# Kernel tuning notes

Hardware: AMD Instinct MI355X
Metric: run time of the kernel (lower is better)

The kernel has to match this reference:

```python
import jax, jax.numpy as jnp
import numpy as np

H = 512

def _lstm_cell(x, h, c, Wih, Whh, bih, bhh):
    # torch LSTM gate order: i, f, g, o
    g = x @ Wih.T + bih + h @ Whh.T + bhh  # (B, 4H)
    i, f, gg, o = jnp.split(g, 4, axis=-1)
    i = jax.nn.sigmoid(i); f = jax.nn.sigmoid(f)
    gg = jnp.tanh(gg);     o = jax.nn.sigmoid(o)
    c_new = f * c + i * gg
    h_new = o * jnp.tanh(c_new)
    return h_new, c_new

def setup_inputs() -> dict:
    key = jax.random.key(0)
    ks = jax.random.split(key, 16)
    B, S, F = 32, 128, 2
    s = 1.0 / np.sqrt(H)
    u = lambda k, shape: jax.random.uniform(k, shape, jnp.float32, -s, s)
    return {
        "inputs": jax.random.normal(ks[0], (B, S, F), jnp.float32),
        "Wp": u(ks[1], (H, F)), "bp": u(ks[2], (H,)),
        "enc_Wih": u(ks[3], (4 * H, H)), "enc_Whh": u(ks[4], (4 * H, H)),
        "enc_bih": u(ks[5], (4 * H,)),   "enc_bhh": u(ks[6], (4 * H,)),
        "dec_Wih": u(ks[7], (4 * H, H)), "dec_Whh": u(ks[8], (4 * H, H)),
        "dec_bih": u(ks[9], (4 * H,)),   "dec_bhh": u(ks[10], (4 * H,)),
        "W1": u(ks[11], (H, H)), "W2": u(ks[12], (H, H)),
        "v": u(ks[13], (H,)),
    }

def reference(inputs, Wp, bp, enc_Wih, enc_Whh, enc_bih, enc_bhh,
              dec_Wih, dec_Whh, dec_bih, dec_bhh, W1, W2, v):
    B, S, _ = inputs.shape
    trg_len = S
    x = inputs @ Wp.T + bp  # (B, S, H) input projection

    # --- encoder LSTM over time ---
    h0 = jnp.zeros((B, H), inputs.dtype)
    c0 = jnp.zeros((B, H), inputs.dtype)
    def enc_step(carry, xt):
        h, c = carry
        h, c = _lstm_cell(xt, h, c, enc_Wih, enc_Whh, enc_bih, enc_bhh)
        return (h, c), h
    (h, c), enc_hs = jax.lax.scan(enc_step, (h0, c0), jnp.swapaxes(x, 0, 1))
    encoder_outputs = jnp.swapaxes(enc_hs, 0, 1)  # (B, S, H)

    # loop-invariant encoder projection (hoisted; identical math)
    enc_proj = encoder_outputs @ W1.T  # (B, S, H)

    # NOTE: the original module never updates its mask (stays all-False),
    # so masking is a no-op and is faithfully omitted.
    dec_in0 = jnp.zeros((B, H), inputs.dtype)
    batch_idx = jnp.arange(B)

    def dec_step(carry, _):
        h, c, dec_in = carry
        h, c = _lstm_cell(dec_in, h, c, dec_Wih, dec_Whh, dec_bih, dec_bhh)
        dec_proj = h @ W2.T  # (B, H)
        scores = jnp.einsum('bsh,h->bs', jnp.tanh(enc_proj + dec_proj[:, None, :]), v)
        log_probs = jax.nn.log_softmax(scores, axis=-1)  # (B, S)
        top_idx = jnp.argmax(log_probs, axis=-1)  # (B,)
        next_in = encoder_outputs[batch_idx, top_idx]  # (B, H)
        return (h, c, next_in), log_probs

    _, all_lp = jax.lax.scan(dec_step, (h, c, dec_in0), None, length=trg_len)
    return jnp.swapaxes(all_lp, 0, 1)  # (B, trg_len, S)
```

## Files before the change

kernel.cpp:

```cpp
#include <hip/hip_runtime.h>
#include <math.h>

static constexpr int H   = 512;
static constexpr int B   = 32;
static constexpr int S   = 128;
static constexpr int G4  = 2048;
static constexpr int UPS = 64;
static constexpr int RPS = 256;
static constexpr int NSL = 8;

static constexpr size_t OFF_E   = 0;
static constexpr size_t SZ_E    = (size_t)B * S * G4;
static constexpr size_t OFF_EO  = OFF_E + SZ_E;
static constexpr size_t SZ_EO   = (size_t)B * S * H;
static constexpr size_t OFF_PT  = OFF_EO + SZ_EO;
static constexpr size_t SZ_PT   = (size_t)B * H * S;
static constexpr size_t OFF_WPE = OFF_PT + SZ_PT;
static constexpr size_t SZ_WP   = (size_t)NSL * H * RPS;
static constexpr size_t OFF_WPD = OFF_WPE + SZ_WP;
static constexpr size_t OFF_W2T = OFF_WPD + SZ_WP;
static constexpr size_t OFF_HB  = OFF_W2T + (size_t)H * H;
static constexpr size_t OFF_CB  = OFF_HB + (size_t)B * 2 * H;
static constexpr size_t OFF_PS  = OFF_CB + (size_t)B * H;
static constexpr size_t OFF_M1  = OFF_PS + (size_t)B * 512;
static constexpr size_t OFF_BE  = OFF_M1 + (size_t)G4 * 2;
static constexpr size_t OFF_DB  = OFF_BE + G4;
static constexpr size_t OFF_END = OFF_DB + G4;
static constexpr int CTRL_U32 = (256 + 256 + 128 + 32) * 32;

__device__ __forceinline__ float sigm(float x){
  float e = __expf(-x);
  return 1.0f / (1.0f + e);
}
__device__ __forceinline__ float tanh_(float x){
  float e = __expf(2.0f * x);
  return 1.0f - 2.0f / (1.0f + e);
}

__device__ __forceinline__ float cloadf(const float* p){
  union { unsigned u; float f; } c;
  c.u = __hip_atomic_load((const unsigned*)p, __ATOMIC_RELAXED,
                          __HIP_MEMORY_SCOPE_AGENT);
  return c.f;
}
__device__ __forceinline__ float2 cload2(const float* p){
  union { unsigned long long u; float2 f; } c;
  c.u = __hip_atomic_load((const unsigned long long*)p, __ATOMIC_RELAXED,
                          __HIP_MEMORY_SCOPE_AGENT);
  return c.f;
}
__device__ __forceinline__ void cstore2(float* p, float a, float b){
  union { unsigned long long u; float2 f; } c;
  c.f = make_float2(a, b);
  __hip_atomic_store((unsigned long long*)p, c.u, __ATOMIC_RELAXED,
                     __HIP_MEMORY_SCOPE_AGENT);
}
__device__ __forceinline__ unsigned cloadu(const unsigned* p){
  return __hip_atomic_load(p, __ATOMIC_RELAXED, __HIP_MEMORY_SCOPE_AGENT);
}
__device__ __forceinline__ void cstoreu(unsigned* p, unsigned v){
  __hip_atomic_store(p, v, __ATOMIC_RELAXED, __HIP_MEMORY_SCOPE_AGENT);
}

__global__ __launch_bounds__(256) void prep_misc(
    const float* __restrict__ eWih, const float* __restrict__ Wp,
    const float* __restrict__ bp,  const float* __restrict__ ebih,
    const float* __restrict__ ebhh, const float* __restrict__ dbih,
    const float* __restrict__ dbhh,
    float* __restrict__ M1, float* __restrict__ bias_e, float* __restrict__ dbias)
{
  int c = blockIdx.x * 256 + threadIdx.x;
  const float* wr = eWih + (size_t)c * H;
  float m0 = 0.f, m1 = 0.f, mb = 0.f;
  for (int k = 0; k < H; k += 4){
    float4 w  = *(const float4*)(wr + k);
    float4 p0 = *(const float4*)(Wp + (size_t)k * 2);
    float4 p1 = *(const float4*)(Wp + (size_t)(k + 2) * 2);
    float4 bb = *(const float4*)(bp + k);
    m0 += w.x*p0.x + w.y*p0.z + w.z*p1.x + w.w*p1.z;
    m1 += w.x*p0.y + w.y*p0.w + w.z*p1.y + w.w*p1.w;
    mb += w.x*bb.x + w.y*bb.y + w.z*bb.z + w.w*bb.w;
  }
  M1[(size_t)c*2]   = m0;
  M1[(size_t)c*2+1] = m1;
  bias_e[c] = ebih[c] + ebhh[c] + mb;
  dbias[c]  = dbih[c] + dbhh[c];
}

__global__ __launch_bounds__(256) void efill(
    const float* __restrict__ inp, const float* __restrict__ M1,
    const float* __restrict__ be, float* __restrict__ E)
{
  size_t i = (size_t)blockIdx.x * 256 + threadIdx.x;
  int c = (int)(i & 2047);
  int t = (int)((i >> 11) & 127);
  int b = (int)(i >> 18);
  float x0 = inp[((size_t)b * S + t) * 2 + 0];
  float x1 = inp[((size_t)b * S + t) * 2 + 1];
  E[i] = M1[(size_t)c*2] * x0 + M1[(size_t)c*2+1] * x1 + be[c];
}

__global__ __launch_bounds__(256) void pack_whh(
    const float* __restrict__ Whh, float* __restrict__ WP)
{
  size_t i = (size_t)blockIdx.x * 256 + threadIdx.x;
  int p = (int)(i & 255);
  int k = (int)((i >> 8) & 511);
  int j = (int)(i >> 17);
  int g = p >> 6, u = p & 63;
  int r = g * 512 + j * UPS + u;
  WP[i] = Whh[(size_t)r * H + k];
}

__global__ __launch_bounds__(256) void transpose_k(
    const float* __restrict__ in, float* __restrict__ out, int R, int K)
{
  __shared__ float tile[32][33];
  int r0 = blockIdx.y * 32, k0 = blockIdx.x * 32;
  int tx = threadIdx.x & 31, ty = threadIdx.x >> 5;
  #pragma unroll
  for (int j = 0; j < 4; ++j)
    tile[ty + 8*j][tx] = in[(size_t)(r0 + ty + 8*j) * K + k0 + tx];
  __syncthreads();
  #pragma unroll
  for (int j = 0; j < 4; ++j)
    out[(size_t)(k0 + ty + 8*j) * R + r0 + tx] = tile[tx][ty + 8*j];
}

template<int LAYOUT>
__global__ __launch_bounds__(256) void gemm_nt(
    const float* __restrict__ A, const float* __restrict__ Bm,
    const float* __restrict__ bias, float* __restrict__ C,
    int M, int N, int K)
{
  __shared__ float As[16][68];
  __shared__ float Bs[16][68];
  int tid = threadIdx.x;
  int bm = blockIdx.y * 64, bn = blockIdx.x * 64;
  int tm = (tid & 15) * 4, tn = (tid >> 4) * 4;
  float acc[4][4] = {};
  int r  = tid >> 2;
  int kq = (tid & 3) * 4;
  for (int k0 = 0; k0 < K; k0 += 16){
    float4 a = *(const float4*)(A  + (size_t)(bm + r) * K + k0 + kq);
    float4 b = *(const float4*)(Bm + (size_t)(bn + r) * K + k0 + kq);
    __syncthreads();
    As[kq+0][r] = a.x; As[kq+1][r] = a.y; As[kq+2][r] = a.z; As[kq+3][r] = a.w;
    Bs[kq+0][r] = b.x; Bs[kq+1][r] = b.y; Bs[kq+2][r] = b.z; Bs[kq+3][r] = b.w;
    __syncthreads();
    #pragma unroll
    for (int kk = 0; kk < 16; ++kk){
      float4 av = *(const float4*)(&As[kk][tm]);
      float4 bv = *(const float4*)(&Bs[kk][tn]);
      acc[0][0] += av.x*bv.x; acc[0][1] += av.x*bv.y; acc[0][2] += av.x*bv.z; acc[0][3] += av.x*bv.w;
      acc[1][0] += av.y*bv.x; acc[1][1] += av.y*bv.y; acc[1][2] += av.y*bv.z; acc[1][3] += av.y*bv.w;
      acc[2][0] += av.z*bv.x; acc[2][1] += av.z*bv.y; acc[2][2] += av.z*bv.z; acc[2][3] += av.z*bv.w;
      acc[3][0] += av.w*bv.x; acc[3][1] += av.w*bv.y; acc[3][2] += av.w*bv.z; acc[3][3] += av.w*bv.w;
    }
  }
  #pragma unroll
  for (int i = 0; i < 4; ++i){
    int m = bm + tm + i;
    #pragma unroll
    for (int j = 0; j < 4; ++j){
      int n = bn + tn + j;
      float vv = acc[i][j] + (bias ? bias[n] : 0.f);
      if (LAYOUT == 0) C[(size_t)m * N + n] = vv;
      else             C[((size_t)(m >> 7) * 512 + n) * 128 + (m & 127)] = vv;
    }
  }
}

__global__ __launch_bounds__(256) void encoder_kernel(
    const float* __restrict__ WP,
    const float* __restrict__ E,
    float* __restrict__ hb,
    float* __restrict__ c_buf,
    float* __restrict__ enc_out,
    unsigned* __restrict__ htags)
{
  __shared__ float hsh[H];
  __shared__ float gpart[4][RPS];
  __shared__ float gfin[4][UPS];
  __shared__ float hloc[UPS];
  const int tid = threadIdx.x, bk = blockIdx.x;
  const int b = bk >> 3, j = bk & 7;
  const int u0 = j * UPS;
  const float* wp = WP + (size_t)j * H * RPS;
  unsigned* myhtags = htags + (size_t)b * 8 * 32;
  const int ph = tid >> 6, c4 = tid & 63;
  float creg = 0.f;
  for (int t = 0; t < S; ++t){
    if (t > 0 && tid < 8){
      while (cloadu(myhtags + tid * 32) < (unsigned)t){}
    }
    __syncthreads();
    { float2 q = cload2(hb + ((size_t)b * 2 + ((t + 1) & 1)) * H + 2 * tid);
      hsh[2*tid] = q.x; hsh[2*tid + 1] = q.y; }
    __syncthreads();
    float4 acc = {0.f, 0.f, 0.f, 0.f};
    const float* wq = wp + ph * RPS + c4 * 4;
    #pragma unroll 4
    for (int kk = 0; kk < 128; ++kk){
      float hv = hsh[4*kk + ph];
      float4 w = *(const float4*)(wq + (size_t)kk * 4 * RPS);
      acc.x = fmaf(w.x, hv, acc.x); acc.y = fmaf(w.y, hv, acc.y);
      acc.z = fmaf(w.z, hv, acc.z); acc.w = fmaf(w.w, hv, acc.w);
    }
    *(float4*)&gpart[ph][c4 * 4] = acc;
    __syncthreads();
    if (tid < 64){
      float4 s0 = *(const float4*)&gpart[0][tid*4];
      float4 s1 = *(const float4*)&gpart[1][tid*4];
      float4 s2 = *(const float4*)&gpart[2][tid*4];
      float4 s3 = *(const float4*)&gpart[3][tid*4];
      int g = tid >> 4, uu = (tid & 15) * 4;
      float4 e = *(const float4*)(E + ((size_t)b * S + t) * G4 + g * 512 + u0 + uu);
      float4 s; s.x = s0.x+s1.x+s2.x+s3.x + e.x; s.y = s0.y+s1.y+s2.y+s3.y + e.y;
      s.z = s0.z+s1.z+s2.z+s3.z + e.z; s.w = s0.w+s1.w+s2.w+s3.w + e.w;
      *(float4*)&gfin[g][uu] = s;
    }
    __syncthreads();
    if (tid < UPS){
      float gi = gfin[0][tid], gf = gfin[1][tid], gg = gfin[2][tid], go = gfin[3][tid];
      creg = sigm(gf) * creg + sigm(gi) * tanh_(gg);
      hloc[tid] = sigm(go) * tanh_(creg);
    }
    __syncthreads();
    if (tid < 32){
      float h0 = hloc[2*tid], h1 = hloc[2*tid + 1];
      cstore2(hb + ((size_t)b * 2 + (t & 1)) * H + u0 + 2*tid, h0, h1);
      *(float2*)(enc_out + ((size_t)b * S + t) * H + u0 + 2*tid) = make_float2(h0, h1);
    }
    __syncthreads();
    if (tid == 0) cstoreu(myhtags + j * 32, (unsigned)(t + 1));
  }
  if (tid < UPS) c_buf[(size_t)b * H + u0 + tid] = creg;
}

__global__ __launch_bounds__(256) void decoder_kernel(
    const float* __restrict__ WP,
    const float* __restrict__ D,
    const float* __restrict__ dbias,
    const float* __restrict__ W2T,
    const float* __restrict__ Pt,
    const float* __restrict__ vvec,
    const float* __restrict__ c_buf,
    const float* __restrict__ enc_out,
    float* __restrict__ hb,
    float* __restrict__ psbuf,
    unsigned* __restrict__ htags,
    unsigned* __restrict__ pstags,
    unsigned* __restrict__ tops,
    float* __restrict__ out)
{
  const int tid = threadIdx.x, bk = blockIdx.x;
  if (bk < 256){
    __shared__ float hsh[H];
    __shared__ float gpart[4][RPS];
    __shared__ float gfin[4][UPS];
    __shared__ float hloc[UPS];
    __shared__ int   topsh;
    const int b = bk >> 3, j = bk & 7;
    const int u0 = j * UPS;
    const float* wp = WP + (size_t)j * H * RPS;
    unsigned* myhtags = htags + (size_t)b * 8 * 32;
    const unsigned* mytop = tops + (size_t)b * 32;
    const int ph = tid >> 6, c4 = tid & 63;
    float creg = (tid < UPS) ? c_buf[(size_t)b * H + u0 + tid] : 0.f;
    if (tid < 32){
      float2 hv = *(const float2*)(enc_out + ((size_t)b * S + (S-1)) * H + u0 + 2*tid);
      cstore2(hb + ((size_t)b * 2 + 1) * H + u0 + 2*tid, hv.x, hv.y);
    }
    __syncthreads();
    if (tid == 0) cstoreu(myhtags + j * 32, 1u);
    for (int t = 0; t < S; ++t){
      if (tid < 8){
        while (cloadu(myhtags + tid * 32) < (unsigned)(t + 1)) __builtin_amdgcn_s_sleep(1);
      }
      __syncthreads();
      { float2 q = cload2(hb + ((size_t)b * 2 + ((t + 1) & 1)) * H + 2 * tid);
        hsh[2*tid] = q.x; hsh[2*tid + 1] = q.y; }
      __syncthreads();
      float4 acc = {0.f, 0.f, 0.f, 0.f};
      const float* wq = wp + ph * RPS + c4 * 4;
      #pragma unroll 4
      for (int kk = 0; kk < 128; ++kk){
        float hv = hsh[4*kk + ph];
        float4 w = *(const float4*)(wq + (size_t)kk * 4 * RPS);
        acc.x = fmaf(w.x, hv, acc.x); acc.y = fmaf(w.y, hv, acc.y);
        acc.z = fmaf(w.z, hv, acc.z); acc.w = fmaf(w.w, hv, acc.w);
      }
      *(float4*)&gpart[ph][c4 * 4] = acc;
      if (t > 0 && tid == 0){
        unsigned vt;
        do { vt = cloadu(mytop); } while ((vt >> 8) != (unsigned)t);
        topsh = (int)(vt & 255u);
      }
      __syncthreads();
      if (tid < 64){
        float4 s0 = *(const float4*)&gpart[0][tid*4];
        float4 s1 = *(const float4*)&gpart[1][tid*4];
        float4 s2 = *(const float4*)&gpart[2][tid*4];
        float4 s3 = *(const float4*)&gpart[3][tid*4];
        int g = tid >> 4, uu = (tid & 15) * 4;
        const float* xr = (t == 0) ? dbias : D + ((size_t)b * S + topsh) * G4;
        float4 e = *(const float4*)(xr + g * 512 + u0 + uu);
        float4 s; s.x = s0.x+s1.x+s2.x+s3.x + e.x; s.y = s0.y+s1.y+s2.y+s3.y + e.y;
        s.z = s0.z+s1.z+s2.z+s3.z + e.z; s.w = s0.w+s1.w+s2.w+s3.w + e.w;
        *(float4*)&gfin[g][uu] = s;
      }
      __syncthreads();
      if (tid < UPS){
        float gi = gfin[0][tid], gf = gfin[1][tid], gg = gfin[2][tid], go = gfin[3][tid];
        creg = sigm(gf) * creg + sigm(gi) * tanh_(gg);
        hloc[tid] = sigm(go) * tanh_(creg);
      }
      __syncthreads();
      if (tid < 32)
        cstore2(hb + ((size_t)b * 2 + (t & 1)) * H + u0 + 2*tid,
                hloc[2*tid], hloc[2*tid + 1]);
      __syncthreads();
      if (tid == 0) cstoreu(myhtags + j * 32, (unsigned)(t + 2));
    }
  } else if (bk < 384){
    __shared__ float hsh[H];
    __shared__ float dps[2][128];
    __shared__ float dpl[128];
    __shared__ float vsh2[128];
    __shared__ float pspart[2][128];
    const int b = (bk - 256) >> 2, q = (bk - 256) & 3;
    const unsigned* myhtags = htags + (size_t)b * 8 * 32;
    unsigned* mytag = pstags + (size_t)(b * 4 + q) * 32;
    if (tid < 128) vsh2[tid] = vvec[q * 128 + tid];
    for (int tau = 0; tau < S; ++tau){
      if (tid < 8){
        while (cloadu(myhtags + tid * 32) < (unsigned)(tau + 2)) __builtin_amdgcn_s_sleep(1);
      }
      __syncthreads();
      { float2 qq = cload2(hb + ((size_t)b * 2 + (tau & 1)) * H + 2 * tid);
        hsh[2*tid] = qq.x; hsh[2*tid + 1] = qq.y; }
      __syncthreads();
      {
        int nl = tid & 127, kh = tid >> 7;
        const float* w = W2T + (size_t)(kh * 256) * H + q * 128 + nl;
        float a = 0.f;
        #pragma unroll 8
        for (int k2 = 0; k2 < 256; ++k2)
          a = fmaf(w[(size_t)k2 * H], hsh[kh * 256 + k2], a);
        dps[kh][nl] = a;
      }
      __syncthreads();
      if (tid < 128) dpl[tid] = dps[0][tid] + dps[1][tid];
      __syncthreads();
      {
        int s = tid & 127, nh = tid >> 7;
        const float* Pp = Pt + ((size_t)b * H + q * 128 + nh * 64) * S + s;
        float cs = 0.f;
        #pragma unroll 4
        for (int n = 0; n < 64; ++n){
          float x = Pp[(size_t)n * S] + dpl[nh * 64 + n];
          cs = fmaf(vsh2[nh * 64 + n], tanh_(x), cs);
        }
        pspart[nh][s] = cs;
      }
      __syncthreads();
      if (tid < 64)
        cstore2(psbuf + ((size_t)b * 4 + q) * 128 + 2 * tid,
                pspart[0][2*tid] + pspart[1][2*tid],
                pspart[0][2*tid+1] + pspart[1][2*tid+1]);
      __syncthreads();
      if (tid == 0) cstoreu(mytag, (unsigned)(tau + 1));
    }
  } else {
    __shared__ float wm[2]; __shared__ int wi[2]; __shared__ float wsum[2];
    const int b = bk - 384;
    unsigned* mytop = tops + (size_t)b * 32;
    for (int t = 0; t < S; ++t){
      if (tid < 4){
        const unsigned* L = pstags + (size_t)(b * 4 + tid) * 32;
        while (cloadu(L) < (unsigned)(t + 1)) __builtin_amdgcn_s_sleep(1);
      }
      __syncthreads();
      float sc = 0.f;
      if (tid < 128){
        const float* pp = psbuf + (size_t)b * 512 + tid;
        sc = cloadf(pp) + cloadf(pp + 128) + cloadf(pp + 256) + cloadf(pp + 384);
        float mv = sc; int mi = tid;
        #pragma unroll
        for (int off = 32; off > 0; off >>= 1){
          float ov = __shfl_xor(mv, off, 64);
          int   oi = __shfl_xor(mi, off, 64);
          if (ov > mv || (ov == mv && oi < mi)){ mv = ov; mi = oi; }
        }
        if ((tid & 63) == 0){ wm[tid >> 6] = mv; wi[tid >> 6] = mi; }
      }
      __syncthreads();
      float mglob; int am;
      { float m0 = wm[0], m1 = wm[1];
        if (m1 > m0 || (m1 == m0 && wi[1] < wi[0])){ mglob = m1; am = wi[1]; }
        else { mglob = m0; am = wi[0]; } }
      if (tid == 0) cstoreu(mytop, ((unsigned)(t + 1) << 8) | (unsigned)am);
      if (tid < 128){
        float se = __expf(sc - mglob);
        float ss = se;
        #pragma unroll
        for (int off = 32; off > 0; off >>= 1) ss += __shfl_xor(ss, off, 64);
        if ((tid & 63) == 0) wsum[tid >> 6] = ss;
      }
      __syncthreads();
      if (tid < 128){
        float lse = __logf(wsum[0] + wsum[1]);
        out[((size_t)b * S + t) * S + tid] = sc - mglob - lse;
      }
      __syncthreads();
    }
  }
}

extern "C" void kernel_launch(void* const* d_in, const int* in_sizes, int n_in,
                              void* d_out, int out_size, void* d_ws, size_t ws_size,
                              hipStream_t stream) {
  const float* inputs  = (const float*)d_in[0];
  const float* Wp      = (const float*)d_in[1];
  const float* bp      = (const float*)d_in[2];
  const float* eWih    = (const float*)d_in[3];
  const float* eWhh    = (const float*)d_in[4];
  const float* ebih    = (const float*)d_in[5];
  const float* ebhh    = (const float*)d_in[6];
  const float* dWih    = (const float*)d_in[7];
  const float* dWhh    = (const float*)d_in[8];
  const float* dbih    = (const float*)d_in[9];
  const float* dbhh    = (const float*)d_in[10];
  const float* W1      = (const float*)d_in[11];
  const float* W2      = (const float*)d_in[12];
  const float* v       = (const float*)d_in[13];
  float* out = (float*)d_out;

  float* ws = (float*)d_ws;
  float* E       = ws + OFF_E;
  float* enc_out = ws + OFF_EO;
  float* Pt      = ws + OFF_PT;
  float* WPe     = ws + OFF_WPE;
  float* WPd     = ws + OFF_WPD;
  float* W2T     = ws + OFF_W2T;
  float* hb      = ws + OFF_HB;
  float* c_buf   = ws + OFF_CB;
  float* psbuf   = ws + OFF_PS;
  float* M1      = ws + OFF_M1;
  float* bias_e  = ws + OFF_BE;
  float* dbias   = ws + OFF_DB;
  unsigned* enc_htags = (unsigned*)(ws + OFF_END);
  unsigned* dec_htags = enc_htags + 256 * 32;
  unsigned* pstags    = dec_htags + 256 * 32;
  unsigned* tops      = pstags + 128 * 32;

  hipMemsetAsync(hb, 0, (size_t)B * 2 * H * sizeof(float), stream);
  hipMemsetAsync(enc_htags, 0, CTRL_U32 * sizeof(unsigned), stream);

  prep_misc<<<G4 / 256, 256, 0, stream>>>(eWih, Wp, bp, ebih, ebhh, dbih, dbhh,
                                          M1, bias_e, dbias);
  efill<<<(int)(SZ_E / 256), 256, 0, stream>>>(inputs, M1, bias_e, E);
  pack_whh<<<(int)(SZ_WP / 256), 256, 0, stream>>>(eWhh, WPe);
  pack_whh<<<(int)(SZ_WP / 256), 256, 0, stream>>>(dWhh, WPd);
  { dim3 g(H / 32, H / 32); transpose_k<<<g, 256, 0, stream>>>(W2, W2T, H, H); }

  encoder_kernel<<<256, 256, 0, stream>>>(WPe, E, hb, c_buf, enc_out, enc_htags);

  float* D = E;
  { dim3 grid(G4 / 64, (B * S) / 64);
    gemm_nt<0><<<grid, 256, 0, stream>>>(enc_out, dWih, dbias, D, B * S, G4, H); }
  { dim3 grid(H / 64, (B * S) / 64);
    gemm_nt<1><<<grid, 256, 0, stream>>>(enc_out, W1, nullptr, Pt, B * S, H, H); }

  decoder_kernel<<<416, 256, 0, stream>>>(WPd, D, dbias, W2T, Pt, v, c_buf,
                                          enc_out, hb, psbuf,
                                          dec_htags, pstags, tops, out);
  (void)in_sizes; (void)n_in; (void)out_size; (void)ws_size;
}
```

Before: 2.959 ms.

## Batch four sequences per block in encoder/decoder to reuse recurrent weights

Each LSTM block now handles four batch rows at once, so every Whh weight slice loaded from memory is reused four times. The encoder grid drops from 256 to 64 blocks and the decoder from 416 to 104. The argmax moves into the LSTM blocks, which read the double-buffered scores themselves, and the log-softmax blocks only write output and signal back through a new tag. This shortens the cross-block dependency chain and cuts weight traffic, but uses far fewer CUs and puts more serial work on each block.

```diff
diff --git a/kernel.cpp b/kernel.cpp
--- a/kernel.cpp
+++ b/kernel.cpp
@@ -8,6 +8,8 @@
 static constexpr int UPS = 64;
 static constexpr int RPS = 256;
 static constexpr int NSL = 8;
+static constexpr int BPG = 4;
+static constexpr int NG  = 8;
 
 static constexpr size_t OFF_E   = 0;
 static constexpr size_t SZ_E    = (size_t)B * S * G4;
@@ -22,11 +24,11 @@
 static constexpr size_t OFF_HB  = OFF_W2T + (size_t)H * H;
 static constexpr size_t OFF_CB  = OFF_HB + (size_t)B * 2 * H;
 static constexpr size_t OFF_PS  = OFF_CB + (size_t)B * H;
-static constexpr size_t OFF_M1  = OFF_PS + (size_t)B * 512;
+static constexpr size_t OFF_M1  = OFF_PS + (size_t)B * 2 * 512;
 static constexpr size_t OFF_BE  = OFF_M1 + (size_t)G4 * 2;
 static constexpr size_t OFF_DB  = OFF_BE + G4;
 static constexpr size_t OFF_END = OFF_DB + G4;
-static constexpr int CTRL_U32 = (256 + 256 + 128 + 32) * 32;
+static constexpr int CTRL_U32 = (64 + 64 + 32 + 8) * 32;
 
 __device__ __forceinline__ float sigm(float x){
   float e = __expf(-x);
@@ -42,6 +44,11 @@
   c.u = __hip_atomic_load((const unsigned*)p, __ATOMIC_RELAXED,
                           __HIP_MEMORY_SCOPE_AGENT);
   return c.f;
+}
+__device__ __forceinline__ void cstoref(float* p, float v){
+  union { unsigned u; float f; } c; c.f = v;
+  __hip_atomic_store((unsigned*)p, c.u, __ATOMIC_RELAXED,
+                     __HIP_MEMORY_SCOPE_AGENT);
 }
 __device__ __forceinline__ float2 cload2(const float* p){
   union { unsigned long long u; float2 f; } c;
@@ -171,6 +178,15 @@
   }
 }
 
+__device__ __forceinline__ void stage_h4(const float* hb, int b0, int par,
+                                         float* hsh, int tid){
+  #pragma unroll
+  for (int bb = 0; bb < BPG; ++bb){
+    float2 q = cload2(hb + ((size_t)(b0 + bb) * 2 + par) * H + 2 * tid);
+    hsh[bb * H + 2 * tid] = q.x; hsh[bb * H + 2 * tid + 1] = q.y;
+  }
+}
+
 __global__ __launch_bounds__(256) void encoder_kernel(
     const float* __restrict__ WP,
     const float* __restrict__ E,
@@ -179,63 +195,55 @@
     float* __restrict__ enc_out,
     unsigned* __restrict__ htags)
 {
-  __shared__ float hsh[H];
-  __shared__ float gpart[4][RPS];
-  __shared__ float gfin[4][UPS];
-  __shared__ float hloc[UPS];
+  __shared__ float hsh[BPG * H];
+  __shared__ float gpart[4][BPG][RPS];
   const int tid = threadIdx.x, bk = blockIdx.x;
-  const int b = bk >> 3, j = bk & 7;
-  const int u0 = j * UPS;
+  const int g = bk >> 3, j = bk & 7;
+  const int b0 = g * BPG, u0 = j * UPS;
   const float* wp = WP + (size_t)j * H * RPS;
-  unsigned* myhtags = htags + (size_t)b * 8 * 32;
+  unsigned* myhtags = htags + (size_t)g * 8 * 32;
   const int ph = tid >> 6, c4 = tid & 63;
+  const int bb = tid >> 6, u = tid & 63;
   float creg = 0.f;
   for (int t = 0; t < S; ++t){
     if (t > 0 && tid < 8){
-      while (cloadu(myhtags + tid * 32) < (unsigned)t){}
-    }
-    __syncthreads();
-    { float2 q = cload2(hb + ((size_t)b * 2 + ((t + 1) & 1)) * H + 2 * tid);
-      hsh[2*tid] = q.x; hsh[2*tid + 1] = q.y; }
-    __syncthreads();
-    float4 acc = {0.f, 0.f, 0.f, 0.f};
+      while (cloadu(myhtags + tid * 32) < (unsigned)t) __builtin_amdgcn_s_sleep(1);
+    }
+    __syncthreads();
+    stage_h4(hb, b0, (t + 1) & 1, hsh, tid);
+    __syncthreads();
+    float4 a0 = {0,0,0,0}, a1 = {0,0,0,0}, a2 = {0,0,0,0}, a3 = {0,0,0,0};
     const float* wq = wp + ph * RPS + c4 * 4;
     #pragma unroll 4
     for (int kk = 0; kk < 128; ++kk){
-      float hv = hsh[4*kk + ph];
+      int k = 4 * kk + ph;
       float4 w = *(const float4*)(wq + (size_t)kk * 4 * RPS);
-      acc.x = fmaf(w.x, hv, acc.x); acc.y = fmaf(w.y, hv, acc.y);
-      acc.z = fmaf(w.z, hv, acc.z); acc.w = fmaf(w.w, hv, acc.w);
-    }
-    *(float4*)&gpart[ph][c4 * 4] = acc;
-    __syncthreads();
-    if (tid < 64){
-      float4 s0 = *(const float4*)&gpart[0][tid*4];
-      float4 s1 = *(const float4*)&gpart[1][tid*4];
-      float4 s2 = *(const float4*)&gpart[2][tid*4];
-      float4 s3 = *(const float4*)&gpart[3][tid*4];
-      int g = tid >> 4, uu = (tid & 15) * 4;
-      float4 e = *(const float4*)(E + ((size_t)b * S + t) * G4 + g * 512 + u0 + uu);
-      float4 s; s.x = s0.x+s1.x+s2.x+s3.x + e.x; s.y = s0.y+s1.y+s2.y+s3.y + e.y;
-      s.z = s0.z+s1.z+s2.z+s3.z + e.z; s.w = s0.w+s1.w+s2.w+s3.w + e.w;
-      *(float4*)&gfin[g][uu] = s;
-    }
-    __syncthreads();
-    if (tid < UPS){
-      float gi = gfin[0][tid], gf = gfin[1][tid], gg = gfin[2][tid], go = gfin[3][tid];
+      float h0 = hsh[k], h1 = hsh[H + k], h2 = hsh[2*H + k], h3 = hsh[3*H + k];
+      a0.x = fmaf(w.x,h0,a0.x); a0.y = fmaf(w.y,h0,a0.y); a0.z = fmaf(w.z,h0,a0.z); a0.w = fmaf(w.w,h0,a0.w);
+      a1.x = fmaf(w.x,h1,a1.x); a1.y = fmaf(w.y,h1,a1.y); a1.z = fmaf(w.z,h1,a1.z); a1.w = fmaf(w.w,h1,a1.w);
+      a2.x = fmaf(w.x,h2,a2.x); a2.y = fmaf(w.y,h2,a2.y); a2.z = fmaf(w.z,h2,a2.z); a2.w = fmaf(w.w,h2,a2.w);
+      a3.x = fmaf(w.x,h3,a3.x); a3.y = fmaf(w.y,h3,a3.y); a3.z = fmaf(w.z,h3,a3.z); a3.w = fmaf(w.w,h3,a3.w);
+    }
+    *(float4*)&gpart[ph][0][c4 * 4] = a0;
+    *(float4*)&gpart[ph][1][c4 * 4] = a1;
+    *(float4*)&gpart[ph][2][c4 * 4] = a2;
+    *(float4*)&gpart[ph][3][c4 * 4] = a3;
+    __syncthreads();
+    {
+      const float* xr = E + ((size_t)(b0 + bb) * S + t) * G4;
+      float gi = gpart[0][bb][      u] + gpart[1][bb][      u] + gpart[2][bb][      u] + gpart[3][bb][      u] + xr[       u0 + u];
+      float gf = gpart[0][bb][ 64 + u] + gpart[1][bb][ 64 + u] + gpart[2][bb][ 64 + u] + gpart[3][bb][ 64 + u] + xr[512  + u0 + u];
+      float gg = gpart[0][bb][128 + u] + gpart[1][bb][128 + u] + gpart[2][bb][128 + u] + gpart[3][bb][128 + u] + xr[1024 + u0 + u];
+      float go = gpart[0][bb][192 + u] + gpart[1][bb][192 + u] + gpart[2][bb][192 + u] + gpart[3][bb][192 + u] + xr[1536 + u0 + u];
       creg = sigm(gf) * creg + sigm(gi) * tanh_(gg);
-      hloc[tid] = sigm(go) * tanh_(creg);
-    }
-    __syncthreads();
-    if (tid < 32){
-      float h0 = hloc[2*tid], h1 = hloc[2*tid + 1];
-      cstore2(hb + ((size_t)b * 2 + (t & 1)) * H + u0 + 2*tid, h0, h1);
-      *(float2*)(enc_out + ((size_t)b * S + t) * H + u0 + 2*tid) = make_float2(h0, h1);
+      float hn = sigm(go) * tanh_(creg);
+      cstoref(hb + ((size_t)(b0 + bb) * 2 + (t & 1)) * H + u0 + u, hn);
+      enc_out[((size_t)(b0 + bb) * S + t) * H + u0 + u] = hn;
     }
     __syncthreads();
     if (tid == 0) cstoreu(myhtags + j * 32, (unsigned)(t + 1));
   }
-  if (tid < UPS) c_buf[(size_t)b * H + u0 + tid] = creg;
+  c_buf[(size_t)(b0 + bb) * H + u0 + u] = creg;
 }
 
 __global__ __launch_bounds__(256) void decoder_kernel(
@@ -251,27 +259,22 @@
     float* __restrict__ psbuf,
     unsigned* __restrict__ htags,
     unsigned* __restrict__ pstags,
-    unsigned* __restrict__ tops,
+    unsigned* __restrict__ otags,
     float* __restrict__ out)
 {
   const int tid = threadIdx.x, bk = blockIdx.x;
-  if (bk < 256){
-    __shared__ float hsh[H];
-    __shared__ float gpart[4][RPS];
-    __shared__ float gfin[4][UPS];
-    __shared__ float hloc[UPS];
-    __shared__ int   topsh;
-    const int b = bk >> 3, j = bk & 7;
-    const int u0 = j * UPS;
+  if (bk < 64){
+    __shared__ float hsh[BPG * H];
+    __shared__ float gpart[4][BPG][RPS];
+    const int g = bk >> 3, j = bk & 7;
+    const int b0 = g * BPG, u0 = j * UPS;
     const float* wp = WP + (size_t)j * H * RPS;
-    unsigned* myhtags = htags + (size_t)b * 8 * 32;
-    const unsigned* mytop = tops + (size_t)b * 32;
+    unsigned* myhtags = htags + (size_t)g * 8 * 32;
     const int ph = tid >> 6, c4 = tid & 63;
-    float creg = (tid < UPS) ? c_buf[(size_t)b * H + u0 + tid] : 0.f;
-    if (tid < 32){
-      float2 hv = *(const float2*)(enc_out + ((size_t)b * S + (S-1)) * H + u0 + 2*tid);
-      cstore2(hb + ((size_t)b * 2 + 1) * H + u0 + 2*tid, hv.x, hv.y);
-    }
+    const int bb = tid >> 6, u = tid & 63;
+    float creg = c_buf[(size_t)(b0 + bb) * H + u0 + u];
+    cstoref(hb + ((size_t)(b0 + bb) * 2 + 1) * H + u0 + u,
+            enc_out[((size_t)(b0 + bb) * S + (S-1)) * H + u0 + u]);
     __syncthreads();
     if (tid == 0) cstoreu(myhtags + j * 32, 1u);
     for (int t = 0; t < S; ++t){
@@ -279,141 +282,157 @@
         while (cloadu(myhtags + tid * 32) < (unsigned)(t + 1)) __builtin_amdgcn_s_sleep(1);
       }
       __syncthreads();
-      { float2 q = cload2(hb + ((size_t)b * 2 + ((t + 1) & 1)) * H + 2 * tid);
-        hsh[2*tid] = q.x; hsh[2*tid + 1] = q.y; }
-      __syncthreads();
-      float4 acc = {0.f, 0.f, 0.f, 0.f};
+      stage_h4(hb, b0, (t + 1) & 1, hsh, tid);
+      __syncthreads();
+      float4 a0 = {0,0,0,0}, a1 = {0,0,0,0}, a2 = {0,0,0,0}, a3 = {0,0,0,0};
       const float* wq = wp + ph * RPS + c4 * 4;
       #pragma unroll 4
       for (int kk = 0; kk < 128; ++kk){
-        float hv = hsh[4*kk + ph];
+        int k = 4 * kk + ph;
         float4 w = *(const float4*)(wq + (size_t)kk * 4 * RPS);
-        acc.x = fmaf(w.x, hv, acc.x); acc.y = fmaf(w.y, hv, acc.y);
-        acc.z = fmaf(w.z, hv, acc.z); acc.w = fmaf(w.w, hv, acc.w);
-      }
-      *(float4*)&gpart[ph][c4 * 4] = acc;
-      if (t > 0 && tid == 0){
-        unsigned vt;
-        do { vt = cloadu(mytop); } while ((vt >> 8) != (unsigned)t);
-        topsh = (int)(vt & 255u);
-      }
-      __syncthreads();
-      if (tid < 64){
-        float4 s0 = *(const float4*)&gpart[0][tid*4];
-        float4 s1 = *(const float4*)&gpart[1][tid*4];
-        float4 s2 = *(const float4*)&gpart[2][tid*4];
-        float4 s3 = *(const float4*)&gpart[3][tid*4];
-        int g = tid >> 4, uu = (tid & 15) * 4;
-        const float* xr = (t == 0) ? dbias : D + ((size_t)b * S + topsh) * G4;
-        float4 e = *(const float4*)(xr + g * 512 + u0 + uu);
-        float4 s; s.x = s0.x+s1.x+s2.x+s3.x + e.x; s.y = s0.y+s1.y+s2.y+s3.y + e.y;
-        s.z = s0.z+s1.z+s2.z+s3.z + e.z; s.w = s0.w+s1.w+s2.w+s3.w + e.w;
-        *(float4*)&gfin[g][uu] = s;
-      }
-      __syncthreads();
-      if (tid < UPS){
-        float gi = gfin[0][tid], gf = gfin[1][tid], gg = gfin[2][tid], go = gfin[3][tid];
-        creg = sigm(gf) * creg + sigm(gi) * tanh_(gg);
-        hloc[tid] = sigm(go) * tanh_(creg);
-      }
-      __syncthreads();
-      if (tid < 32)
-        cstore2(hb + ((size_t)b * 2 + (t & 1)) * H + u0 + 2*tid,
-                hloc[2*tid], hloc[2*tid + 1]);
-      __syncthreads();
-      if (tid == 0) cstoreu(myhtags + j * 32, (unsigned)(t + 2));
-    }
-  } else if (bk < 384){
-    __shared__ float hsh[H];
-    __shared__ float dps[2][128];
-    __shared__ float dpl[128];
-    __shared__ float vsh2[128];
-    __shared__ float pspart[2][128];
-    const int b = (bk - 256) >> 2, q = (bk - 256) & 3;
-    const unsigned* myhtags = htags + (size_t)b * 8 * 32;
-    unsigned* mytag = pstags + (size_t)(b * 4 + q) * 32;
-    if (tid < 128) vsh2[tid] = vvec[q * 128 + tid];
-    for (int tau = 0; tau < S; ++tau){
-      if (tid < 8){
-        while (cloadu(myhtags + tid * 32) < (unsigned)(tau + 2)) __builtin_amdgcn_s_sleep(1);
-      }
-      __syncthreads();
-      { float2 qq = cload2(hb + ((size_t)b * 2 + (tau & 1)) * H + 2 * tid);
-        hsh[2*tid] = qq.x; hsh[2*tid + 1] = qq.y; }
-      __syncthreads();
-      {
-        int nl = tid & 127, kh = tid >> 7;
-        const float* w = W2T + (size_t)(kh * 256) * H + q * 128 + nl;
-        float a = 0.f;
-        #pragma unroll 8
-        for (int k2 = 0; k2 < 256; ++k2)
-          a = fmaf(w[(size_t)k2 * H], hsh[kh * 256 + k2], a);
-        dps[kh][nl] = a;
-      }
-      __syncthreads();
-      if (tid < 128) dpl[tid] = dps[0][tid] + dps[1][tid];
-      __syncthreads();
-      {
-        int s = tid & 127, nh = tid >> 7;
-        const float* Pp = Pt + ((size_t)b * H + q * 128 + nh * 64) * S + s;
-        float cs = 0.f;
-        #pragma unroll 4
-        for (int n = 0; n < 64; ++n){
-          float x = Pp[(size_t)n * S] + dpl[nh * 64 + n];
-          cs = fmaf(vsh2[nh * 64 + n], tanh_(x), cs);
-        }
-        pspart[nh][s] = cs;
-      }
-      __syncthreads();
-      if (tid < 64)
-        cstore2(psbuf + ((size_t)b * 4 + q) * 128 + 2 * tid,
-                pspart[0][2*tid] + pspart[1][2*tid],
-                pspart[0][2*tid+1] + pspart[1][2*tid+1]);
-      __syncthreads();
-      if (tid == 0) cstoreu(mytag, (unsigned)(tau + 1));
-    }
-  } else {
-    __shared__ float wm[2]; __shared__ int wi[2]; __shared__ float wsum[2];
-    const int b = bk - 384;
-    unsigned* mytop = tops + (size_t)b * 32;
-    for (int t = 0; t < S; ++t){
-      if (tid < 4){
-        const unsigned* L = pstags + (size_t)(b * 4 + tid) * 32;
-        while (cloadu(L) < (unsigned)(t + 1)) __builtin_amdgcn_s_sleep(1);
-      }
-      __syncthreads();
-      float sc = 0.f;
-      if (tid < 128){
-        const float* pp = psbuf + (size_t)b * 512 + tid;
-        sc = cloadf(pp) + cloadf(pp + 128) + cloadf(pp + 256) + cloadf(pp + 384);
-        float mv = sc; int mi = tid;
+        float h0 = hsh[k], h1 = hsh[H + k], h2 = hsh[2*H + k], h3 = hsh[3*H + k];
+        a0.x = fmaf(w.x,h0,a0.x); a0.y = fmaf(w.y,h0,a0.y); a0.z = fmaf(w.z,h0,a0.z); a0.w = fmaf(w.w,h0,a0.w);
+        a1.x = fmaf(w.x,h1,a1.x); a1.y = fmaf(w.y,h1,a1.y); a1.z = fmaf(w.z,h1,a1.z); a1.w = fmaf(w.w,h1,a1.w);
+        a2.x = fmaf(w.x,h2,a2.x); a2.y = fmaf(w.y,h2,a2.y); a2.z = fmaf(w.z,h2,a2.z); a2.w = fmaf(w.w,h2,a2.w);
+        a3.x = fmaf(w.x,h3,a3.x); a3.y = fmaf(w.y,h3,a3.y); a3.z = fmaf(w.z,h3,a3.z); a3.w = fmaf(w.w,h3,a3.w);
+      }
+      *(float4*)&gpart[ph][0][c4 * 4] = a0;
+      *(float4*)&gpart[ph][1][c4 * 4] = a1;
+      *(float4*)&gpart[ph][2][c4 * 4] = a2;
+      *(float4*)&gpart[ph][3][c4 * 4] = a3;
+      if (t >= 1 && tid < 4){
+        while (cloadu(pstags + (size_t)(g * 4 + tid) * 32) < (unsigned)t)
+          __builtin_amdgcn_s_sleep(1);
+      }
+      __syncthreads();
+      int top = 0;
+      if (t >= 1){
+        const float* pp = psbuf + ((size_t)(b0 + bb) * 2 + ((t + 1) & 1)) * 512;
+        float s0 = cloadf(pp + u)       + cloadf(pp + 128 + u)
+                 + cloadf(pp + 256 + u) + cloadf(pp + 384 + u);
+        float s1 = cloadf(pp + 64 + u)  + cloadf(pp + 192 + u)
+                 + cloadf(pp + 320 + u) + cloadf(pp + 448 + u);
+        float mv; int mi;
+        if (s1 > s0){ mv = s1; mi = u + 64; } else { mv = s0; mi = u; }
         #pragma unroll
         for (int off = 32; off > 0; off >>= 1){
           float ov = __shfl_xor(mv, off, 64);
           int   oi = __shfl_xor(mi, off, 64);
           if (ov > mv || (ov == mv && oi < mi)){ mv = ov; mi = oi; }
         }
-        if ((tid & 63) == 0){ wm[tid >> 6] = mv; wi[tid >> 6] = mi; }
-      }
-      __syncthreads();
-      float mglob; int am;
-      { float m0 = wm[0], m1 = wm[1];
-        if (m1 > m0 || (m1 == m0 && wi[1] < wi[0])){ mglob = m1; am = wi[1]; }
-        else { mglob = m0; am = wi[0]; } }
-      if (tid == 0) cstoreu(mytop, ((unsigned)(t + 1) << 8) | (unsigned)am);
-      if (tid < 128){
-        float se = __expf(sc - mglob);
-        float ss = se;
+        top = mi;
+      }
+      {
+        const float* xr = (t == 0) ? dbias
+                                   : D + ((size_t)(b0 + bb) * S + top) * G4;
+        float gi = gpart[0][bb][      u] + gpart[1][bb][      u] + gpart[2][bb][      u] + gpart[3][bb][      u] + xr[       u0 + u];
+        float gf = gpart[0][bb][ 64 + u] + gpart[1][bb][ 64 + u] + gpart[2][bb][ 64 + u] + gpart[3][bb][ 64 + u] + xr[512  + u0 + u];
+        float gg = gpart[0][bb][128 + u] + gpart[1][bb][128 + u] + gpart[2][bb][128 + u] + gpart[3][bb][128 + u] + xr[1024 + u0 + u];
+        float go = gpart[0][bb][192 + u] + gpart[1][bb][192 + u] + gpart[2][bb][192 + u] + gpart[3][bb][192 + u] + xr[1536 + u0 + u];
+        creg = sigm(gf) * creg + sigm(gi) * tanh_(gg);
+        float hn = sigm(go) * tanh_(creg);
+        cstoref(hb + ((size_t)(b0 + bb) * 2 + (t & 1)) * H + u0 + u, hn);
+      }
+      __syncthreads();
+      if (tid == 0) cstoreu(myhtags + j * 32, (unsigned)(t + 2));
+    }
+  } else if (bk < 96){
+    __shared__ float hsh[BPG * H];
+    __shared__ float dps[2][BPG][128];
+    __shared__ float dpl[BPG][128];
+    __shared__ float vsh[128];
+    __shared__ float psps[BPG][128];
+    const int idx = bk - 64;
+    const int g = idx >> 2, q = idx & 3;
+    const int b0 = g * BPG;
+    unsigned* myhtags = htags + (size_t)g * 8 * 32;
+    unsigned* mytag = pstags + (size_t)(g * 4 + q) * 32;
+    const unsigned* myotag = otags + (size_t)g * 32;
+    if (tid < 128) vsh[tid] = vvec[q * 128 + tid];
+    for (int tau = 0; tau < S; ++tau){
+      if (tid < 8){
+        while (cloadu(myhtags + tid * 32) < (unsigned)(tau + 2)) __builtin_amdgcn_s_sleep(1);
+      } else if (tid == 8 && tau >= 2){
+        while (cloadu(myotag) < (unsigned)(tau - 1)) __builtin_amdgcn_s_sleep(1);
+      }
+      __syncthreads();
+      stage_h4(hb, b0, tau & 1, hsh, tid);
+      __syncthreads();
+      {
+        int nl = tid & 127, kh = tid >> 7;
+        const float* w = W2T + (size_t)(kh * 256) * H + q * 128 + nl;
+        float d0 = 0.f, d1 = 0.f, d2 = 0.f, d3 = 0.f;
+        const float* h0p = hsh + kh * 256;
+        #pragma unroll 8
+        for (int k2 = 0; k2 < 256; ++k2){
+          float wv = w[(size_t)k2 * H];
+          d0 = fmaf(wv, h0p[k2],         d0);
+          d1 = fmaf(wv, h0p[H + k2],     d1);
+          d2 = fmaf(wv, h0p[2*H + k2],   d2);
+          d3 = fmaf(wv, h0p[3*H + k2],   d3);
+        }
+        dps[kh][0][nl] = d0; dps[kh][1][nl] = d1;
+        dps[kh][2][nl] = d2; dps[kh][3][nl] = d3;
+      }
+      __syncthreads();
+      { int w2 = tid;        dpl[w2 >> 7][w2 & 127] = dps[0][w2 >> 7][w2 & 127] + dps[1][w2 >> 7][w2 & 127];
+        w2 = tid + 256;      dpl[w2 >> 7][w2 & 127] = dps[0][w2 >> 7][w2 & 127] + dps[1][w2 >> 7][w2 & 127]; }
+      __syncthreads();
+      {
+        int s = tid & 127, pair = tid >> 7;
         #pragma unroll
-        for (int off = 32; off > 0; off >>= 1) ss += __shfl_xor(ss, off, 64);
-        if ((tid & 63) == 0) wsum[tid >> 6] = ss;
-      }
-      __syncthreads();
-      if (tid < 128){
-        float lse = __logf(wsum[0] + wsum[1]);
-        out[((size_t)b * S + t) * S + tid] = sc - mglob - lse;
-      }
-      __syncthreads();
+        for (int e = 0; e < 2; ++e){
+          int bb = pair + 2 * e;
+          const float* Pp = Pt + ((size_t)(b0 + bb) * H + q * 128) * S + s;
+          const float* dq = dpl[bb];
+          float cs = 0.f;
+          #pragma unroll 4
+          for (int n = 0; n < 128; ++n){
+            float x = Pp[(size_t)n * S] + dq[n];
+            cs = fmaf(vsh[n], tanh_(x), cs);
+          }
+          psps[bb][s] = cs;
+        }
+      }
+      __syncthreads();
+      {
+        int bb = tid >> 6, i = tid & 63;
+        cstore2(psbuf + ((size_t)(b0 + bb) * 2 + (tau & 1)) * 512 + q * 128 + 2 * i,
+                psps[bb][2*i], psps[bb][2*i + 1]);
+      }
+      __syncthreads();
+      if (tid == 0) cstoreu(mytag, (unsigned)(tau + 1));
+    }
+  } else {
+    const int g = bk - 96;
+    const int b0 = g * BPG;
+    unsigned* myotag = otags + (size_t)g * 32;
+    const int bb = tid >> 6, u = tid & 63;
+    for (int t = 0; t < S; ++t){
+      if (tid < 4){
+        while (cloadu(pstags + (size_t)(g * 4 + tid) * 32) < (unsigned)(t + 1))
+          __builtin_amdgcn_s_sleep(1);
+      }
+      __syncthreads();
+      const float* pp = psbuf + ((size_t)(b0 + bb) * 2 + (t & 1)) * 512;
+      float s0 = cloadf(pp + u)       + cloadf(pp + 128 + u)
+               + cloadf(pp + 256 + u) + cloadf(pp + 384 + u);
+      float s1 = cloadf(pp + 64 + u)  + cloadf(pp + 192 + u)
+               + cloadf(pp + 320 + u) + cloadf(pp + 448 + u);
+      float mv = fmaxf(s0, s1);
+      #pragma unroll
+      for (int off = 32; off > 0; off >>= 1)
+        mv = fmaxf(mv, __shfl_xor(mv, off, 64));
+      float ss = __expf(s0 - mv) + __expf(s1 - mv);
+      #pragma unroll
+      for (int off = 32; off > 0; off >>= 1)
+        ss += __shfl_xor(ss, off, 64);
+      float lse = __logf(ss);
+      float* orow = out + ((size_t)(b0 + bb) * S + t) * S;
+      orow[u]      = s0 - mv - lse;
+      orow[64 + u] = s1 - mv - lse;
+      __syncthreads();
+      if (tid == 0) cstoreu(myotag, (unsigned)(t + 1));
     }
   }
 }
@@ -451,9 +470,9 @@
   float* bias_e  = ws + OFF_BE;
   float* dbias   = ws + OFF_DB;
   unsigned* enc_htags = (unsigned*)(ws + OFF_END);
-  unsigned* dec_htags = enc_htags + 256 * 32;
-  unsigned* pstags    = dec_htags + 256 * 32;
-  unsigned* tops      = pstags + 128 * 32;
+  unsigned* dec_htags = enc_htags + 64 * 32;
+  unsigned* pstags    = dec_htags + 64 * 32;
+  unsigned* otags     = pstags + 32 * 32;
 
   hipMemsetAsync(hb, 0, (size_t)B * 2 * H * sizeof(float), stream);
   hipMemsetAsync(enc_htags, 0, CTRL_U32 * sizeof(unsigned), stream);
@@ -465,7 +484,7 @@
   pack_whh<<<(int)(SZ_WP / 256), 256, 0, stream>>>(dWhh, WPd);
   { dim3 g(H / 32, H / 32); transpose_k<<<g, 256, 0, stream>>>(W2, W2T, H, H); }
 
-  encoder_kernel<<<256, 256, 0, stream>>>(WPe, E, hb, c_buf, enc_out, enc_htags);
+  encoder_kernel<<<64, 256, 0, stream>>>(WPe, E, hb, c_buf, enc_out, enc_htags);
 
   float* D = E;
   { dim3 grid(G4 / 64, (B * S) / 64);
@@ -473,8 +492,8 @@
   { dim3 grid(H / 64, (B * S) / 64);
     gemm_nt<1><<<grid, 256, 0, stream>>>(enc_out, W1, nullptr, Pt, B * S, H, H); }
 
-  decoder_kernel<<<416, 256, 0, stream>>>(WPd, D, dbias, W2T, Pt, v, c_buf,
+  decoder_kernel<<<104, 256, 0, stream>>>(WPd, D, dbias, W2T, Pt, v, c_buf,
                                           enc_out, hb, psbuf,
-                                          dec_htags, pstags, tops, out);
+                                          dec_htags, pstags, otags, out);
   (void)in_sizes; (void)n_in; (void)out_size; (void)ws_size;
 }
```

Result: slower. 4.733 ms (+59.9%).

## Compute argmax redundantly in LSTM blocks to remove a cross-block handoff hop

Applied to the files above, without the earlier changes.

Each decoder LSTM block now reads the four partial score slices and does its own argmax, instead of waiting on a top-index tag published by a separate softmax block. This removes one inter-block signalling hop from the serial per-step critical path. The score buffer is double-buffered, and the score blocks now wait on a new output tag from the softmax block so a buffer is not overwritten before it is read. The cost is redundant argmax work across 8 blocks per batch row and extra polling.

```diff
diff --git a/kernel.cpp b/kernel.cpp
--- a/kernel.cpp
+++ b/kernel.cpp
@@ -22,7 +22,7 @@
 static constexpr size_t OFF_HB  = OFF_W2T + (size_t)H * H;
 static constexpr size_t OFF_CB  = OFF_HB + (size_t)B * 2 * H;
 static constexpr size_t OFF_PS  = OFF_CB + (size_t)B * H;
-static constexpr size_t OFF_M1  = OFF_PS + (size_t)B * 512;
+static constexpr size_t OFF_M1  = OFF_PS + (size_t)B * 2 * 512;
 static constexpr size_t OFF_BE  = OFF_M1 + (size_t)G4 * 2;
 static constexpr size_t OFF_DB  = OFF_BE + G4;
 static constexpr size_t OFF_END = OFF_DB + G4;
@@ -251,7 +251,7 @@
     float* __restrict__ psbuf,
     unsigned* __restrict__ htags,
     unsigned* __restrict__ pstags,
-    unsigned* __restrict__ tops,
+    unsigned* __restrict__ otags,
     float* __restrict__ out)
 {
   const int tid = threadIdx.x, bk = blockIdx.x;
@@ -260,12 +260,11 @@
     __shared__ float gpart[4][RPS];
     __shared__ float gfin[4][UPS];
     __shared__ float hloc[UPS];
-    __shared__ int   topsh;
+    __shared__ float wm[2]; __shared__ int wi[2];
     const int b = bk >> 3, j = bk & 7;
     const int u0 = j * UPS;
     const float* wp = WP + (size_t)j * H * RPS;
     unsigned* myhtags = htags + (size_t)b * 8 * 32;
-    const unsigned* mytop = tops + (size_t)b * 32;
     const int ph = tid >> 6, c4 = tid & 63;
     float creg = (tid < UPS) ? c_buf[(size_t)b * H + u0 + tid] : 0.f;
     if (tid < 32){
@@ -292,19 +291,34 @@
         acc.z = fmaf(w.z, hv, acc.z); acc.w = fmaf(w.w, hv, acc.w);
       }
       *(float4*)&gpart[ph][c4 * 4] = acc;
-      if (t > 0 && tid == 0){
-        unsigned vt;
-        do { vt = cloadu(mytop); } while ((vt >> 8) != (unsigned)t);
-        topsh = (int)(vt & 255u);
-      }
-      __syncthreads();
+      if (t >= 1 && tid < 4){
+        while (cloadu(pstags + (size_t)(b * 4 + tid) * 32) < (unsigned)t)
+          __builtin_amdgcn_s_sleep(1);
+      }
+      __syncthreads();
+      if (t >= 1 && tid < 128){
+        const float* pp = psbuf + ((size_t)b * 2 + ((t + 1) & 1)) * 512 + tid;
+        float sc = cloadf(pp) + cloadf(pp + 128) + cloadf(pp + 256) + cloadf(pp + 384);
+        float mv = sc; int mi = tid;
+        #pragma unroll
+        for (int off = 32; off > 0; off >>= 1){
+          float ov = __shfl_xor(mv, off, 64);
+          int   oi = __shfl_xor(mi, off, 64);
+          if (ov > mv || (ov == mv && oi < mi)){ mv = ov; mi = oi; }
+        }
+        if ((tid & 63) == 0){ wm[tid >> 6] = mv; wi[tid >> 6] = mi; }
+      }
+      __syncthreads();
+      int top = 0;
+      if (t >= 1)
+        top = (wm[1] > wm[0] || (wm[1] == wm[0] && wi[1] < wi[0])) ? wi[1] : wi[0];
       if (tid < 64){
         float4 s0 = *(const float4*)&gpart[0][tid*4];
         float4 s1 = *(const float4*)&gpart[1][tid*4];
         float4 s2 = *(const float4*)&gpart[2][tid*4];
         float4 s3 = *(const float4*)&gpart[3][tid*4];
         int g = tid >> 4, uu = (tid & 15) * 4;
-        const float* xr = (t == 0) ? dbias : D + ((size_t)b * S + topsh) * G4;
+        const float* xr = (t == 0) ? dbias : D + ((size_t)b * S + top) * G4;
         float4 e = *(const float4*)(xr + g * 512 + u0 + uu);
         float4 s; s.x = s0.x+s1.x+s2.x+s3.x + e.x; s.y = s0.y+s1.y+s2.y+s3.y + e.y;
         s.z = s0.z+s1.z+s2.z+s3.z + e.z; s.w = s0.w+s1.w+s2.w+s3.w + e.w;
@@ -332,10 +346,13 @@
     const int b = (bk - 256) >> 2, q = (bk - 256) & 3;
     const unsigned* myhtags = htags + (size_t)b * 8 * 32;
     unsigned* mytag = pstags + (size_t)(b * 4 + q) * 32;
+    const unsigned* myotag = otags + (size_t)b * 32;
     if (tid < 128) vsh2[tid] = vvec[q * 128 + tid];
     for (int tau = 0; tau < S; ++tau){
       if (tid < 8){
         while (cloadu(myhtags + tid * 32) < (unsigned)(tau + 2)) __builtin_amdgcn_s_sleep(1);
+      } else if (tid == 8 && tau >= 2){
+        while (cloadu(myotag) < (unsigned)(tau - 1)) __builtin_amdgcn_s_sleep(1);
       }
       __syncthreads();
       { float2 qq = cload2(hb + ((size_t)b * 2 + (tau & 1)) * H + 2 * tid);
@@ -366,44 +383,36 @@
       }
       __syncthreads();
       if (tid < 64)
-        cstore2(psbuf + ((size_t)b * 4 + q) * 128 + 2 * tid,
+        cstore2(psbuf + ((size_t)b * 2 + (tau & 1)) * 512 + q * 128 + 2 * tid,
                 pspart[0][2*tid] + pspart[1][2*tid],
                 pspart[0][2*tid+1] + pspart[1][2*tid+1]);
       __syncthreads();
       if (tid == 0) cstoreu(mytag, (unsigned)(tau + 1));
     }
   } else {
-    __shared__ float wm[2]; __shared__ int wi[2]; __shared__ float wsum[2];
+    __shared__ float wm2[2]; __shared__ float wsum[2];
     const int b = bk - 384;
-    unsigned* mytop = tops + (size_t)b * 32;
+    unsigned* myotag = otags + (size_t)b * 32;
     for (int t = 0; t < S; ++t){
       if (tid < 4){
-        const unsigned* L = pstags + (size_t)(b * 4 + tid) * 32;
-        while (cloadu(L) < (unsigned)(t + 1)) __builtin_amdgcn_s_sleep(1);
+        while (cloadu(pstags + (size_t)(b * 4 + tid) * 32) < (unsigned)(t + 1))
+          __builtin_amdgcn_s_sleep(1);
       }
       __syncthreads();
       float sc = 0.f;
       if (tid < 128){
-        const float* pp = psbuf + (size_t)b * 512 + tid;
+        const float* pp = psbuf + ((size_t)b * 2 + (t & 1)) * 512 + tid;
         sc = cloadf(pp) + cloadf(pp + 128) + cloadf(pp + 256) + cloadf(pp + 384);
-        float mv = sc; int mi = tid;
+        float mv = sc;
         #pragma unroll
-        for (int off = 32; off > 0; off >>= 1){
-          float ov = __shfl_xor(mv, off, 64);
-          int   oi = __shfl_xor(mi, off, 64);
-          if (ov > mv || (ov == mv && oi < mi)){ mv = ov; mi = oi; }
-        }
-        if ((tid & 63) == 0){ wm[tid >> 6] = mv; wi[tid >> 6] = mi; }
-      }
-      __syncthreads();
-      float mglob; int am;
-      { float m0 = wm[0], m1 = wm[1];
-        if (m1 > m0 || (m1 == m0 && wi[1] < wi[0])){ mglob = m1; am = wi[1]; }
-        else { mglob = m0; am = wi[0]; } }
-      if (tid == 0) cstoreu(mytop, ((unsigned)(t + 1) << 8) | (unsigned)am);
+        for (int off = 32; off > 0; off >>= 1)
+          mv = fmaxf(mv, __shfl_xor(mv, off, 64));
+        if ((tid & 63) == 0) wm2[tid >> 6] = mv;
+      }
+      __syncthreads();
+      float mglob = fmaxf(wm2[0], wm2[1]);
       if (tid < 128){
-        float se = __expf(sc - mglob);
-        float ss = se;
+        float ss = __expf(sc - mglob);
         #pragma unroll
         for (int off = 32; off > 0; off >>= 1) ss += __shfl_xor(ss, off, 64);
         if ((tid & 63) == 0) wsum[tid >> 6] = ss;
@@ -414,6 +423,7 @@
         out[((size_t)b * S + t) * S + tid] = sc - mglob - lse;
       }
       __syncthreads();
+      if (tid == 0) cstoreu(myotag, (unsigned)(t + 1));
     }
   }
 }
@@ -453,7 +463,7 @@
   unsigned* enc_htags = (unsigned*)(ws + OFF_END);
   unsigned* dec_htags = enc_htags + 256 * 32;
   unsigned* pstags    = dec_htags + 256 * 32;
-  unsigned* tops      = pstags + 128 * 32;
+  unsigned* otags     = pstags + 128 * 32;
 
   hipMemsetAsync(hb, 0, (size_t)B * 2 * H * sizeof(float), stream);
   hipMemsetAsync(enc_htags, 0, CTRL_U32 * sizeof(unsigned), stream);
@@ -475,6 +485,6 @@
 
   decoder_kernel<<<416, 256, 0, stream>>>(WPd, D, dbias, W2T, Pt, v, c_buf,
                                           enc_out, hb, psbuf,
-                                          dec_htags, pstags, tops, out);
+                                          dec_htags, pstags, otags, out);
   (void)in_sizes; (void)n_in; (void)out_size; (void)ws_size;
 }
```

Result: no change. 2.933 ms (-0.9%).
